# Optimization experiments

Measured on AMD Instinct MI355X. Metric: run time of the kernel, lower is better.

Reference implementation:

```python
import jax, jax.numpy as jnp
import numpy as np

NUM_ENT_CLASS = 150
NORMED_REL_VEC_DIST = False


def box_cxcywh_to_xyxy(b):
    cx, cy, w, h = b[..., 0], b[..., 1], b[..., 2], b[..., 3]
    return jnp.stack([cx - 0.5 * w, cy - 0.5 * h, cx + 0.5 * w, cy + 0.5 * h], axis=-1)


def box_xyxy_to_cxcywh(b):
    x0, y0, x1, y1 = b[..., 0], b[..., 1], b[..., 2], b[..., 3]
    return jnp.stack([(x0 + x1) * 0.5, (y0 + y1) * 0.5, x1 - x0, y1 - y0], axis=-1)


def generalized_box_iou(a, b):
    # a: [N,4], b: [M,4], xyxy -> [N,M]
    area_a = (a[:, 2] - a[:, 0]) * (a[:, 3] - a[:, 1])
    area_b = (b[:, 2] - b[:, 0]) * (b[:, 3] - b[:, 1])
    lt = jnp.maximum(a[:, None, :2], b[None, :, :2])
    rb = jnp.minimum(a[:, None, 2:], b[None, :, 2:])
    wh = jnp.clip(rb - lt, 0.0)
    inter = wh[..., 0] * wh[..., 1]
    union = area_a[:, None] + area_b[None, :] - inter
    iou = inter / union
    lt_c = jnp.minimum(a[:, None, :2], b[None, :, :2])
    rb_c = jnp.maximum(a[:, None, 2:], b[None, :, 2:])
    wh_c = jnp.clip(rb_c - lt_c, 0.0)
    area_c = wh_c[..., 0] * wh_c[..., 1]
    return iou - (area_c - union) / area_c


def cdist_l2(a, b):
    # a: [N,C], b: [M,C] -> [N,M] euclidean distance (gram-matrix form)
    d2 = (jnp.sum(a * a, -1)[:, None] + jnp.sum(b * b, -1)[None, :]
          - 2.0 * (a @ b.T))
    return jnp.sqrt(jnp.maximum(d2, 1e-12))


def _per_image(ent_box_n, ent_logits, ro_logits, rs_logits, ro_box_n, rs_box_n,
               rel_vec_n, scale):
    # scale: [4] = [w, h, w, h]
    ent_box = box_cxcywh_to_xyxy(ent_box_n) * scale[None, :]           # [Ne,4] pixels
    ent_cnter = box_xyxy_to_cxcywh(ent_box)[..., :2]                    # [Ne,2]
    ent_cnter_normed = ent_box_n[..., :2]

    # num_ent_class (150) != logits dim (151) -> softmax, drop background
    ro_dist = jax.nn.softmax(ro_logits, axis=-1)[..., :-1]              # [Nr,150]
    rs_dist = jax.nn.softmax(rs_logits, axis=-1)[..., :-1]
    ent_prob = jax.nn.softmax(ent_logits, axis=-1)[..., :-1]            # [Ne,150]
    ent_score = jnp.max(ent_prob, axis=-1)                              # [Ne]

    ro_box = box_cxcywh_to_xyxy(ro_box_n) * scale[None, :]              # [Nr,4]
    rs_box = box_cxcywh_to_xyxy(rs_box_n) * scale[None, :]
    rel_vec = rel_vec_n * scale[None, :]                                # [Nr,4]

    if NORMED_REL_VEC_DIST:
        vec, sc, oc = rel_vec_n, ent_cnter_normed, ent_cnter_normed
    else:
        vec, sc, oc = rel_vec, ent_cnter, ent_cnter

    # L1 distance of rel-vector endpoints to entity centers -> [Nr,Ne]
    dist_s = (jnp.abs(vec[:, None, 0] - sc[None, :, 0])
              + jnp.abs(vec[:, None, 1] - sc[None, :, 1]))
    dist_o = (jnp.abs(vec[:, None, 2] - oc[None, :, 0])
              + jnp.abs(vec[:, None, 3] - oc[None, :, 1]))
    match_vec_sub = 1.0 / (dist_s + 1.0)
    match_vec_obj = 1.0 / (dist_o + 1.0)

    m_s = ent_score[None, :] * match_vec_sub                            # conf-weighted
    m_o = ent_score[None, :] * match_vec_obj

    sub_giou = jnp.clip(generalized_box_iou(ent_box, rs_box), 0.0)      # [Ne,Nr]
    obj_giou = jnp.clip(generalized_box_iou(ent_box, ro_box), 0.0)

    sub_cls = 1.0 / (cdist_l2(rs_dist, ent_prob) + 1.0)                 # [Nr,Ne]
    obj_cls = 1.0 / (cdist_l2(ro_dist, ent_prob) + 1.0)

    dist_s_final = m_s * sub_cls * sub_giou.T                           # [Nr,Ne]
    dist_o_final = m_o * obj_cls * obj_giou.T
    return dist_s_final, dist_o_final


def setup_inputs() -> dict:
    key = jax.random.key(0)
    ks = jax.random.split(key, 8)
    B, Ne, Nr, C1 = 64, 500, 500, NUM_ENT_CLASS + 1
    inp = {
        "pred_boxes": jax.random.uniform(ks[0], (B, Ne, 4), jnp.float32),
        "pred_logits": jax.random.normal(ks[1], (B, Ne, C1), jnp.float32),
        "pred_rel_obj_logits": jax.random.normal(ks[2], (B, Nr, C1), jnp.float32),
        "pred_rel_sub_logits": jax.random.normal(ks[3], (B, Nr, C1), jnp.float32),
        "pred_rel_obj_box": jax.random.uniform(ks[4], (B, Nr, 4), jnp.float32),
        "pred_rel_sub_box": jax.random.uniform(ks[5], (B, Nr, 4), jnp.float32),
        "pred_rel_vec": jax.random.uniform(ks[6], (B, Nr, 4), jnp.float32),
        "target_sizes": 600.0 + 600.0 * jax.random.uniform(ks[7], (B, 2), jnp.float32),
    }
    return inp


def reference(pred_boxes, pred_logits, pred_rel_obj_logits, pred_rel_sub_logits,
              pred_rel_obj_box, pred_rel_sub_box, pred_rel_vec, target_sizes):
    img_h, img_w = target_sizes[:, 0], target_sizes[:, 1]
    scale_fct = jnp.stack([img_w, img_h, img_w, img_h], axis=1)  # [B,4]
    sub_dist, obj_dist = jax.vmap(_per_image)(
        pred_boxes, pred_logits, pred_rel_obj_logits, pred_rel_sub_logits,
        pred_rel_obj_box, pred_rel_sub_box, pred_rel_vec, scale_fct)
    return sub_dist, obj_dist
```

## Files before the change

### kernel.cpp

```cpp
#include <hip/hip_runtime.h>
#include <math.h>

#define NB   64
#define NPT  500
#define C1   151
#define CM1  150
#define EAF  12
#define RAF  20

#define GRP_ELEMS  2560
#define IMG_ELEMS  (32 * GRP_ELEMS)
#define PROB_ELEMS ((size_t)NB * IMG_ELEMS)

typedef __bf16 bf16x8 __attribute__((ext_vector_type(8)));
typedef float  f32x4  __attribute__((ext_vector_type(4)));

__device__ __forceinline__ float rcpf(float x) { return __builtin_amdgcn_rcpf(x); }
__device__ __forceinline__ float rsqf(float x) { return __builtin_amdgcn_rsqf(x); }

extern "C" __global__ void __launch_bounds__(256)
k_pre(const float* __restrict__ boxes, const float* __restrict__ ent_logits,
      const float* __restrict__ ro_logits, const float* __restrict__ rs_logits,
      const float* __restrict__ ro_box, const float* __restrict__ rs_box,
      const float* __restrict__ rel_vec, const float* __restrict__ tsz,
      __bf16* __restrict__ entP, __bf16* __restrict__ rsP, __bf16* __restrict__ roP,
      float* __restrict__ entAux, float* __restrict__ relAux)
{
    const int tid = threadIdx.x;
    const int q   = tid & 15;
    const int rl  = tid >> 4;
    const int bx  = blockIdx.x;
    const int set = bx / 2000;
    const int rowIdx = (bx - set * 2000) * 16 + rl;
    const int b = rowIdx / 500;
    const int i = rowIdx - b * 500;

    const float* src = (set == 0 ? ent_logits : (set == 1 ? rs_logits : ro_logits))
                       + (size_t)rowIdx * C1;

    float x[10];
    #pragma unroll
    for (int t = 0; t < 9; ++t) x[t] = src[q + 16 * t];
    x[9] = (q <= 6) ? src[q + 144] : -INFINITY;

    float mAll = x[0];
    #pragma unroll
    for (int t = 1; t < 10; ++t) mAll = fmaxf(mAll, x[t]);
    float mKept = x[0];
    #pragma unroll
    for (int t = 1; t < 9; ++t) mKept = fmaxf(mKept, x[t]);
    if (q <= 5) mKept = fmaxf(mKept, x[9]);

    #pragma unroll
    for (int off = 1; off < 16; off <<= 1) {
        mAll  = fmaxf(mAll,  __shfl_xor(mAll,  off, 16));
        mKept = fmaxf(mKept, __shfl_xor(mKept, off, 16));
    }

    float e[10], s = 0.f, s2 = 0.f;
    #pragma unroll
    for (int t = 0; t < 9; ++t) {
        e[t] = __expf(x[t] - mAll);
        s  += e[t];
        s2 += e[t] * e[t];
    }
    e[9] = (q <= 6) ? __expf(x[9] - mAll) : 0.f;
    s += e[9];
    if (q <= 5) s2 += e[9] * e[9];

    #pragma unroll
    for (int off = 1; off < 16; off <<= 1) {
        s  += __shfl_xor(s,  off, 16);
        s2 += __shfl_xor(s2, off, 16);
    }

    const float inv = rcpf(s);
    const float pm  = __expf(mKept - mAll) * inv;
    const float nn  = s2 * inv * inv;

    __bf16* dstT = (set == 0 ? entP : (set == 1 ? rsP : roP));
    const int g  = i >> 4, ir = i & 15;
    __bf16* dst = dstT + ((size_t)b * 32 + g) * GRP_ELEMS + ir * 8 + (q & 7);
    const int qh = q >> 3;
    #pragma unroll
    for (int t = 0; t < 9; ++t)
        dst[(2 * t + qh) * 128] = (__bf16)(e[t] * inv);
    dst[(18 + qh) * 128] = (q <= 5) ? (__bf16)(e[9] * inv) : (__bf16)0.f;

    if (q == 0) {
        const float hh = tsz[b * 2 + 0];
        const float ww = tsz[b * 2 + 1];
        if (set == 0) {
            const float* bb = boxes + (size_t)rowIdx * 4;
            const float cx = bb[0], cy = bb[1], bw = bb[2], bh = bb[3];
            const float X0 = (cx - 0.5f * bw) * ww, Y0 = (cy - 0.5f * bh) * hh;
            const float X1 = (cx + 0.5f * bw) * ww, Y1 = (cy + 0.5f * bh) * hh;
            float* A = entAux + (size_t)rowIdx * EAF;
            A[0] = pm;
            A[1] = 0.5f * (X0 + X1);
            A[2] = 0.5f * (Y0 + Y1);
            A[3] = nn;
            A[4] = X0; A[5] = Y0; A[6] = X1; A[7] = Y1;
            A[8] = (X1 - X0) * (Y1 - Y0);
        } else if (set == 1) {
            const float* bb = rs_box  + (size_t)rowIdx * 4;
            const float* vv = rel_vec + (size_t)rowIdx * 4;
            const float cx = bb[0], cy = bb[1], bw = bb[2], bh = bb[3];
            float* A = relAux + (size_t)rowIdx * RAF;
            const float X0 = (cx - 0.5f * bw) * ww, Y0 = (cy - 0.5f * bh) * hh;
            const float X1 = (cx + 0.5f * bw) * ww, Y1 = (cy + 0.5f * bh) * hh;
            A[0] = X0; A[1] = Y0; A[2] = X1; A[3] = Y1;
            A[8]  = vv[0] * ww; A[9]  = vv[1] * hh;
            A[10] = vv[2] * ww; A[11] = vv[3] * hh;
            A[12] = nn;
            A[14] = (X1 - X0) * (Y1 - Y0);
        } else {
            const float* bb = ro_box + (size_t)rowIdx * 4;
            const float cx = bb[0], cy = bb[1], bw = bb[2], bh = bb[3];
            float* A = relAux + (size_t)rowIdx * RAF;
            const float X0 = (cx - 0.5f * bw) * ww, Y0 = (cy - 0.5f * bh) * hh;
            const float X1 = (cx + 0.5f * bw) * ww, Y1 = (cy + 0.5f * bh) * hh;
            A[4] = X0; A[5] = Y0; A[6] = X1; A[7] = Y1;
            A[13] = nn;
            A[15] = (X1 - X0) * (Y1 - Y0);
        }
    }
}

template <bool FULL>
__device__ __forceinline__ void epilogue(
    const float (*eA)[EAF], const float (*rA)[RAF],
    const f32x4* accS, const f32x4* accO,
    int lr, int kq, int wv, int b, int e0T, int r0T,
    float* __restrict__ outS, float* __restrict__ outO)
{
    f32x4 ev0[4], ev1[4];
    float eArea[4];
    #pragma unroll
    for (int et = 0; et < 4; ++et) {
        const float* ep = eA[et * 16 + lr];
        ev0[et] = *(const f32x4*)(ep);
        ev1[et] = *(const f32x4*)(ep + 4);
        eArea[et] = ep[8];
    }

    const unsigned baseR0 = ((unsigned)b * NPT + (unsigned)(r0T + wv * 16 + kq * 4)) * NPT;
    const unsigned eBase  = (unsigned)(e0T + lr);

    #pragma unroll
    for (int reg = 0; reg < 4; ++reg) {
        const int rIdx = wv * 16 + kq * 4 + reg;
        const bool rOK = FULL || (r0T + rIdx < NPT);
        const float* rp = rA[rIdx];
        const f32x4 rsB = *(const f32x4*)(rp);
        const f32x4 roB = *(const f32x4*)(rp + 4);
        const f32x4 vv  = *(const f32x4*)(rp + 8);
        const f32x4 rn  = *(const f32x4*)(rp + 12);
        const unsigned rowOff = baseR0 + (unsigned)reg * NPT;

        #pragma unroll
        for (int et = 0; et < 4; ++et) {
            const float score = ev0[et][0], ecx = ev0[et][1], ecy = ev0[et][2], en2 = ev0[et][3];
            const float ex0 = ev1[et][0], ey0 = ev1[et][1], ex1 = ev1[et][2], ey1 = ev1[et][3];
            const float aE = eArea[et];

            const float iwS = fmaxf(fminf(ex1, rsB[2]) - fmaxf(ex0, rsB[0]), 0.f);
            const float ihS = fmaxf(fminf(ey1, rsB[3]) - fmaxf(ey0, rsB[1]), 0.f);
            const float inS = iwS * ihS;
            const float unS = aE + rn[2] - inS;
            const float aCS = (fmaxf(ex1, rsB[2]) - fminf(ex0, rsB[0]))
                            * (fmaxf(ey1, rsB[3]) - fminf(ey0, rsB[1]));
            const float gS  = fmaxf(fmaf(fmaf(inS, aCS, unS * unS), rcpf(unS * aCS), -1.f), 0.f);

            const float iwO = fmaxf(fminf(ex1, roB[2]) - fmaxf(ex0, roB[0]), 0.f);
            const float ihO = fmaxf(fminf(ey1, roB[3]) - fmaxf(ey0, roB[1]), 0.f);
            const float inO = iwO * ihO;
            const float unO = aE + rn[3] - inO;
            const float aCO = (fmaxf(ex1, roB[2]) - fminf(ex0, roB[0]))
                            * (fmaxf(ey1, roB[3]) - fminf(ey0, roB[1]));
            const float gO  = fmaxf(fmaf(fmaf(inO, aCO, unO * unO), rcpf(unO * aCO), -1.f), 0.f);

            const float d2s = fmaxf(fmaf(-2.f, accS[et][reg], rn[0] + en2), 1e-12f);
            const float d2o = fmaxf(fmaf(-2.f, accO[et][reg], rn[1] + en2), 1e-12f);
            const float dS  = d2s * rsqf(d2s);
            const float dO  = d2o * rsqf(d2o);
            const float distS = fabsf(vv[0] - ecx) + fabsf(vv[1] - ecy);
            const float distO = fabsf(vv[2] - ecx) + fabsf(vv[3] - ecy);
            const float qS = rcpf((distS + 1.f) * (dS + 1.f));
            const float qO = rcpf((distO + 1.f) * (dO + 1.f));

            const float vS = score * qS * gS;
            const float vO = score * qO * gO;

            const unsigned o = rowOff + eBase + (unsigned)(et * 16);
            if (FULL || (rOK && (int)(eBase + et * 16) < NPT)) {
                outS[o] = vS;
                outO[o] = vO;
            }
        }
    }
}

extern "C" __global__ void __launch_bounds__(256, 4)
k_main(const __bf16* __restrict__ entP, const __bf16* __restrict__ rsP,
       const __bf16* __restrict__ roP, const float* __restrict__ eAuxG,
       const float* __restrict__ rAuxG,
       float* __restrict__ outS, float* __restrict__ outO)
{
    __shared__ __align__(16) __bf16 sEnt[4 * GRP_ELEMS];
    __shared__ __align__(16) float eA[64][EAF];
    __shared__ __align__(16) float rA[64][RAF];

    const int tid = threadIdx.x;
    const int b   = blockIdx.x;
    const int e0T = (blockIdx.y & 7) * 64;
    const int r0T = (blockIdx.y >> 3) * 64;

    const int wv   = tid >> 6;
    const int lane = tid & 63;
    const int lr   = lane & 15;
    const int kq   = lane >> 4;

    const int gR = (r0T >> 4) + wv;
    const int gE = (e0T >> 4);
    const __bf16* rsBase = rsP  + ((size_t)b * 32 + gR) * GRP_ELEMS + lr * 8;
    const __bf16* roBase = roP  + ((size_t)b * 32 + gR) * GRP_ELEMS + lr * 8;
    const __bf16* entSrc = entP + ((size_t)b * 32 + gE) * GRP_ELEMS;

    bf16x8 ars[5], aro[5];
    #pragma unroll
    for (int ks = 0; ks < 5; ++ks) {
        const int kOff = (ks * 4 + kq) * 128;
        ars[ks] = *(const bf16x8*)(rsBase + kOff);
        aro[ks] = *(const bf16x8*)(roBase + kOff);
    }

    #pragma unroll
    for (int it = 0; it < 5; ++it) {
        const int off = it * 4096 + wv * 1024;
        __builtin_amdgcn_global_load_lds(
            (const __attribute__((address_space(1))) unsigned int*)
                ((const char*)entSrc + off + lane * 16),
            (__attribute__((address_space(3))) unsigned int*)
                ((char*)sEnt + off),
            16, 0, 0);
    }

    {
        const float4 z = {0.f, 0.f, 0.f, 0.f};
        for (int t = tid; t < 64 * (EAF / 4); t += 256) {
            const int e = t / (EAF / 4), qq = t % (EAF / 4);
            const int ge = e0T + e;
            ((float4*)eA[e])[qq] = (ge < NPT)
                ? ((const float4*)(eAuxG + ((size_t)b * NPT + ge) * EAF))[qq] : z;
        }
        for (int t = tid; t < 64 * (RAF / 4); t += 256) {
            const int r = t / (RAF / 4), qq = t % (RAF / 4);
            const int gr = r0T + r;
            ((float4*)rA[r])[qq] = (gr < NPT)
                ? ((const float4*)(rAuxG + ((size_t)b * NPT + gr) * RAF))[qq] : z;
        }
    }
    __syncthreads();

    f32x4 accS[4] = {{0,0,0,0},{0,0,0,0},{0,0,0,0},{0,0,0,0}};
    f32x4 accO[4] = {{0,0,0,0},{0,0,0,0},{0,0,0,0},{0,0,0,0}};

    #pragma unroll
    for (int ks = 0; ks < 5; ++ks) {
        const int kOff = (ks * 4 + kq) * 128 + lr * 8;
        #pragma unroll
        for (int et = 0; et < 4; ++et) {
            const bf16x8 be = *(const bf16x8*)&sEnt[et * GRP_ELEMS + kOff];
            accS[et] = __builtin_amdgcn_mfma_f32_16x16x32_bf16(ars[ks], be, accS[et], 0, 0, 0);
            accO[et] = __builtin_amdgcn_mfma_f32_16x16x32_bf16(aro[ks], be, accO[et], 0, 0, 0);
        }
    }

    if (e0T + 64 <= NPT && r0T + 64 <= NPT) {
        epilogue<true >(eA, rA, accS, accO, lr, kq, wv, b, e0T, r0T, outS, outO);
    } else {
        epilogue<false>(eA, rA, accS, accO, lr, kq, wv, b, e0T, r0T, outS, outO);
    }
}

extern "C" void kernel_launch(void* const* d_in, const int* in_sizes, int n_in,
                              void* d_out, int out_size, void* d_ws, size_t ws_size,
                              hipStream_t stream)
{
    const float* boxes      = (const float*)d_in[0];
    const float* ent_logits = (const float*)d_in[1];
    const float* ro_logits  = (const float*)d_in[2];
    const float* rs_logits  = (const float*)d_in[3];
    const float* ro_box     = (const float*)d_in[4];
    const float* rs_box     = (const float*)d_in[5];
    const float* rel_vec    = (const float*)d_in[6];
    const float* tsz        = (const float*)d_in[7];

    __bf16* entP = (__bf16*)d_ws;
    __bf16* rsP  = entP + PROB_ELEMS;
    __bf16* roP  = rsP  + PROB_ELEMS;
    float*  eAux = (float*)(roP + PROB_ELEMS);
    float*  rAux = eAux + (size_t)NB * NPT * EAF;

    float* outS = (float*)d_out;
    float* outO = outS + (size_t)NB * NPT * NPT;

    hipLaunchKernelGGL(k_pre, dim3(6000), dim3(256), 0, stream,
                       boxes, ent_logits, ro_logits, rs_logits,
                       ro_box, rs_box, rel_vec, tsz,
                       entP, rsP, roP, eAux, rAux);

    hipLaunchKernelGGL(k_main, dim3(64, 64), dim3(256), 0, stream,
                       entP, rsP, roP, eAux, rAux, outS, outO);
}
```

Measured before the change: 235.0 us.

## Loop each block over four relation tiles, reusing the staged entity tile

Each k_main block now stages one 64-entity probability tile in LDS and walks four 64-row relation tiles in sequence, so the grid shrinks from 64x64 to 64x16 blocks. Entity aux data is read once into registers, and relation aux data is read straight from global memory inside the epilogue instead of being staged through LDS. This cuts redundant entity-tile loads and per-block setup. In exchange there are fewer blocks to hide latency, the relation loops run serially with no prefetch overlap, and aux reads become uncoalesced.

```diff
diff --git a/kernel.cpp b/kernel.cpp
--- a/kernel.cpp
+++ b/kernel.cpp
@@ -129,29 +129,21 @@
 
 template <bool FULL>
 __device__ __forceinline__ void epilogue(
-    const float (*eA)[EAF], const float (*rA)[RAF],
+    const f32x4* ev0, const f32x4* ev1, const float* eArea,
+    const float* __restrict__ rAuxG,
     const f32x4* accS, const f32x4* accO,
     int lr, int kq, int wv, int b, int e0T, int r0T,
     float* __restrict__ outS, float* __restrict__ outO)
 {
-    f32x4 ev0[4], ev1[4];
-    float eArea[4];
-    #pragma unroll
-    for (int et = 0; et < 4; ++et) {
-        const float* ep = eA[et * 16 + lr];
-        ev0[et] = *(const f32x4*)(ep);
-        ev1[et] = *(const f32x4*)(ep + 4);
-        eArea[et] = ep[8];
-    }
-
     const unsigned baseR0 = ((unsigned)b * NPT + (unsigned)(r0T + wv * 16 + kq * 4)) * NPT;
     const unsigned eBase  = (unsigned)(e0T + lr);
 
     #pragma unroll
     for (int reg = 0; reg < 4; ++reg) {
         const int rIdx = wv * 16 + kq * 4 + reg;
-        const bool rOK = FULL || (r0T + rIdx < NPT);
-        const float* rp = rA[rIdx];
+        const int gr   = r0T + rIdx;
+        const bool rOK = FULL || (gr < NPT);
+        const float* rp = rAuxG + ((size_t)b * NPT + gr) * RAF;
         const f32x4 rsB = *(const f32x4*)(rp);
         const f32x4 roB = *(const f32x4*)(rp + 4);
         const f32x4 vv  = *(const f32x4*)(rp + 8);
@@ -208,33 +200,18 @@
        float* __restrict__ outS, float* __restrict__ outO)
 {
     __shared__ __align__(16) __bf16 sEnt[4 * GRP_ELEMS];
-    __shared__ __align__(16) float eA[64][EAF];
-    __shared__ __align__(16) float rA[64][RAF];
 
     const int tid = threadIdx.x;
     const int b   = blockIdx.x;
-    const int e0T = (blockIdx.y & 7) * 64;
-    const int r0T = (blockIdx.y >> 3) * 64;
+    const int e0T = (blockIdx.y & 1) * 64 + (blockIdx.y >> 2) * 128;
+    const int rS  = ((blockIdx.y >> 1) & 1) * 256;
 
     const int wv   = tid >> 6;
     const int lane = tid & 63;
     const int lr   = lane & 15;
     const int kq   = lane >> 4;
 
-    const int gR = (r0T >> 4) + wv;
-    const int gE = (e0T >> 4);
-    const __bf16* rsBase = rsP  + ((size_t)b * 32 + gR) * GRP_ELEMS + lr * 8;
-    const __bf16* roBase = roP  + ((size_t)b * 32 + gR) * GRP_ELEMS + lr * 8;
-    const __bf16* entSrc = entP + ((size_t)b * 32 + gE) * GRP_ELEMS;
-
-    bf16x8 ars[5], aro[5];
-    #pragma unroll
-    for (int ks = 0; ks < 5; ++ks) {
-        const int kOff = (ks * 4 + kq) * 128;
-        ars[ks] = *(const bf16x8*)(rsBase + kOff);
-        aro[ks] = *(const bf16x8*)(roBase + kOff);
-    }
-
+    const __bf16* entSrc = entP + ((size_t)b * 32 + (e0T >> 4)) * GRP_ELEMS;
     #pragma unroll
     for (int it = 0; it < 5; ++it) {
         const int off = it * 4096 + wv * 1024;
@@ -246,41 +223,53 @@
             16, 0, 0);
     }
 
-    {
-        const float4 z = {0.f, 0.f, 0.f, 0.f};
-        for (int t = tid; t < 64 * (EAF / 4); t += 256) {
-            const int e = t / (EAF / 4), qq = t % (EAF / 4);
-            const int ge = e0T + e;
-            ((float4*)eA[e])[qq] = (ge < NPT)
-                ? ((const float4*)(eAuxG + ((size_t)b * NPT + ge) * EAF))[qq] : z;
-        }
-        for (int t = tid; t < 64 * (RAF / 4); t += 256) {
-            const int r = t / (RAF / 4), qq = t % (RAF / 4);
-            const int gr = r0T + r;
-            ((float4*)rA[r])[qq] = (gr < NPT)
-                ? ((const float4*)(rAuxG + ((size_t)b * NPT + gr) * RAF))[qq] : z;
-        }
+    f32x4 ev0[4], ev1[4];
+    float eArea[4];
+    #pragma unroll
+    for (int et = 0; et < 4; ++et) {
+        const float* ep = eAuxG + ((size_t)b * NPT + e0T + et * 16 + lr) * EAF;
+        ev0[et] = *(const f32x4*)(ep);
+        ev1[et] = *(const f32x4*)(ep + 4);
+        eArea[et] = ep[8];
     }
     __syncthreads();
 
-    f32x4 accS[4] = {{0,0,0,0},{0,0,0,0},{0,0,0,0},{0,0,0,0}};
-    f32x4 accO[4] = {{0,0,0,0},{0,0,0,0},{0,0,0,0},{0,0,0,0}};
-
-    #pragma unroll
-    for (int ks = 0; ks < 5; ++ks) {
-        const int kOff = (ks * 4 + kq) * 128 + lr * 8;
+    const bool fullE = (e0T + 64 <= NPT);
+
+    #pragma unroll 1
+    for (int rt = 0; rt < 4; ++rt) {
+        const int r0T = rS + rt * 64;
+        const int gR  = (r0T >> 4) + wv;
+        const __bf16* rsBase = rsP + ((size_t)b * 32 + gR) * GRP_ELEMS + lr * 8;
+        const __bf16* roBase = roP + ((size_t)b * 32 + gR) * GRP_ELEMS + lr * 8;
+
+        bf16x8 ars[5], aro[5];
         #pragma unroll
-        for (int et = 0; et < 4; ++et) {
-            const bf16x8 be = *(const bf16x8*)&sEnt[et * GRP_ELEMS + kOff];
-            accS[et] = __builtin_amdgcn_mfma_f32_16x16x32_bf16(ars[ks], be, accS[et], 0, 0, 0);
-            accO[et] = __builtin_amdgcn_mfma_f32_16x16x32_bf16(aro[ks], be, accO[et], 0, 0, 0);
-        }
-    }
-
-    if (e0T + 64 <= NPT && r0T + 64 <= NPT) {
-        epilogue<true >(eA, rA, accS, accO, lr, kq, wv, b, e0T, r0T, outS, outO);
-    } else {
-        epilogue<false>(eA, rA, accS, accO, lr, kq, wv, b, e0T, r0T, outS, outO);
+        for (int ks = 0; ks < 5; ++ks) {
+            const int kOff = (ks * 4 + kq) * 128;
+            ars[ks] = *(const bf16x8*)(rsBase + kOff);
+            aro[ks] = *(const bf16x8*)(roBase + kOff);
+        }
+
+        f32x4 accS[4] = {{0,0,0,0},{0,0,0,0},{0,0,0,0},{0,0,0,0}};
+        f32x4 accO[4] = {{0,0,0,0},{0,0,0,0},{0,0,0,0},{0,0,0,0}};
+
+        #pragma unroll
+        for (int ks = 0; ks < 5; ++ks) {
+            const int kOff = (ks * 4 + kq) * 128 + lr * 8;
+            #pragma unroll
+            for (int et = 0; et < 4; ++et) {
+                const bf16x8 be = *(const bf16x8*)&sEnt[et * GRP_ELEMS + kOff];
+                accS[et] = __builtin_amdgcn_mfma_f32_16x16x32_bf16(ars[ks], be, accS[et], 0, 0, 0);
+                accO[et] = __builtin_amdgcn_mfma_f32_16x16x32_bf16(aro[ks], be, accO[et], 0, 0, 0);
+            }
+        }
+
+        if (fullE && r0T + 64 <= NPT) {
+            epilogue<true >(ev0, ev1, eArea, rAuxG, accS, accO, lr, kq, wv, b, e0T, r0T, outS, outO);
+        } else {
+            epilogue<false>(ev0, ev1, eArea, rAuxG, accS, accO, lr, kq, wv, b, e0T, r0T, outS, outO);
+        }
     }
 }
 
@@ -311,6 +300,6 @@
                        ro_box, rs_box, rel_vec, tsz,
                        entP, rsP, roP, eAux, rAux);
 
-    hipLaunchKernelGGL(k_main, dim3(64, 64), dim3(256), 0, stream,
+    hipLaunchKernelGGL(k_main, dim3(64, 16), dim3(256), 0, stream,
                        entP, rsP, roP, eAux, rAux, outS, outO);
 }
```

After: 328.8 us. +39.9%, slower.
